# Kernel optimization log

Measured on AMD Instinct MI355X. Metric: run time of the kernel, lower is better.

Reference implementation:

```python
import jax, jax.numpy as jnp
import numpy as np

B, S, H = 32, 512, 1024


def setup_inputs() -> dict:
    key = jax.random.key(0)
    ks = jax.random.split(key, 8)
    scale = 1.0 / np.sqrt(H)
    x = jax.random.normal(ks[0], (B, S, H), dtype=jnp.float32)
    # realistic padding: each sequence has a valid length in [S//2, S]; 1 = masked
    lengths = jax.random.randint(ks[1], (B,), S // 2, S + 1)
    padding_mask = (jnp.arange(S)[None, :] >= lengths[:, None]).astype(jnp.float32)
    def w(k, shape):
        return (jax.random.normal(k, shape, dtype=jnp.float32) * scale).astype(jnp.float32)
    W_fw = w(ks[2], (H, 4 * H))
    U_fw = w(ks[3], (H, 4 * H))
    b_fw = jnp.zeros((4 * H,), jnp.float32)
    W_bw = w(ks[4], (H, 4 * H))
    U_bw = w(ks[5], (H, 4 * H))
    b_bw = jnp.zeros((4 * H,), jnp.float32)
    return {"src_token_embeddings": x, "padding_mask": padding_mask,
            "W_fw": W_fw, "U_fw": U_fw, "b_fw": b_fw,
            "W_bw": W_bw, "U_bw": U_bw, "b_bw": b_bw}


def _lstm_dir(x, mask, W, U, b):
    """Masked LSTM over time (Keras semantics: masked steps carry state and
    repeat the previous output). x: [B,S,H], mask: [B,S] with 1 = keep."""
    Bx, Sx, Hx = x.shape
    xz = jnp.einsum('bsh,hg->bsg', x, W) + b          # [B,S,4H] precomputed input gates
    xz_t = jnp.transpose(xz, (1, 0, 2))               # [S,B,4H]
    m_t = jnp.transpose(mask, (1, 0))[:, :, None]     # [S,B,1]
    h0 = jnp.zeros((Bx, Hx), x.dtype)

    def step(carry, inp):
        h, c, out_prev = carry
        z, m = inp
        z = z + h @ U                                  # [B,4H]
        i, f, g, o = jnp.split(z, 4, axis=-1)
        i = jax.nn.sigmoid(i)
        f = jax.nn.sigmoid(f)
        g = jnp.tanh(g)
        o = jax.nn.sigmoid(o)
        c_new = f * c + i * g
        h_new = o * jnp.tanh(c_new)
        h2 = m * h_new + (1.0 - m) * h
        c2 = m * c_new + (1.0 - m) * c
        out = m * h_new + (1.0 - m) * out_prev
        return (h2, c2, out), out

    (hT, cT, _), outs = jax.lax.scan(step, (h0, h0, h0), (xz_t, m_t))
    return jnp.transpose(outs, (1, 0, 2)), hT, cT


def reference(src_token_embeddings, padding_mask, W_fw, U_fw, b_fw, W_bw, U_bw, b_bw):
    x = src_token_embeddings
    mask = 1.0 - padding_mask                          # 1 = keep, as in the Keras call
    out_fw, h_fw, c_fw = _lstm_dir(x, mask, W_fw, U_fw, b_fw)
    # backward direction: process time-reversed sequence, then reverse outputs back
    out_bw_rev, h_bw, c_bw = _lstm_dir(x[:, ::-1], mask[:, ::-1], W_bw, U_bw, b_bw)
    out_bw = out_bw_rev[:, ::-1]
    encoder_outputs = jnp.concatenate([out_fw, out_bw], axis=-1)  # [B,S,2H]
    return encoder_outputs, h_fw, c_fw, h_bw, c_bw
```

## Files before the change

kernel.cpp:

```cpp
#include <hip/hip_runtime.h>
#include <hip/hip_bf16.h>

#define B 32
#define S 512
#define H 1024
#define G 4096
#define NBLK 256
#define HSLOT 65536

typedef __attribute__((ext_vector_type(8))) short bf16x8;
typedef __attribute__((ext_vector_type(8))) unsigned short u16x8;
typedef __attribute__((ext_vector_type(4))) float f32x4;

__device__ __forceinline__ unsigned short f2bf(float v) {
    __hip_bfloat16 b = __float2bfloat16(v);
    return *reinterpret_cast<unsigned short*>(&b);
}
__device__ __forceinline__ float bf2f(unsigned short u) {
    union { float f; unsigned int i; } v; v.i = ((unsigned int)u) << 16; return v.f;
}
#define MFMA(a, b, c) __builtin_amdgcn_mfma_f32_16x16x32_bf16(a, b, c, 0, 0, 0)
#define ALOAD(p)    __hip_atomic_load((p),  __ATOMIC_RELAXED, __HIP_MEMORY_SCOPE_AGENT)
#define ASTORE(p,v) __hip_atomic_store((p), (v), __ATOMIC_RELAXED, __HIP_MEMORY_SCOPE_AGENT)

__global__ __launch_bounds__(256)
void prep_weights(const float* __restrict__ fw, const float* __restrict__ bw,
                  unsigned short* __restrict__ dst)
{
    size_t idx = (size_t)blockIdx.x * 256 + threadIdx.x;
    int lane = idx & 63;
    int f    = (idx >> 6) & 15;
    int w    = (idx >> 10) & 3;
    int blk  = (int)(idx >> 12);
    int dir  = blk >> 7, jg = blk & 127;
    int ks = f >> 1, ct = f & 1;

    int c  = ct * 16 + (lane & 15);
    int g  = (c >> 3) * H + jg * 8 + (c & 7);
    int kk = w * 256 + ks * 32 + ((lane >> 4) * 8);

    const float* src = dir ? bw : fw;
    u16x8 o;
#pragma unroll
    for (int i = 0; i < 8; ++i)
        o[i] = f2bf(src[(size_t)(kk + i) * G + g]);
    *(u16x8*)&dst[idx * 8] = o;
}

__global__ __launch_bounds__(256)
void prep_x(const float* __restrict__ x, unsigned short* __restrict__ xbf)
{
    size_t i8 = ((size_t)blockIdx.x * 256 + threadIdx.x) * 8;
    float4 v0 = *(const float4*)&x[i8];
    float4 v1 = *(const float4*)&x[i8 + 4];
    u16x8 o;
    o[0] = f2bf(v0.x); o[1] = f2bf(v0.y); o[2] = f2bf(v0.z); o[3] = f2bf(v0.w);
    o[4] = f2bf(v1.x); o[5] = f2bf(v1.y); o[6] = f2bf(v1.z); o[7] = f2bf(v1.w);
    *(u16x8*)&xbf[i8] = o;
}

__global__ __launch_bounds__(512, 1)
void lstm_persist(const unsigned short* __restrict__ wbufU,
                  const unsigned short* __restrict__ wbufW,
                  const unsigned short* __restrict__ xbf,
                  unsigned short* __restrict__ hhist,
                  unsigned int* __restrict__ flags,
                  unsigned int* __restrict__ gen,
                  const float* __restrict__ pad,
                  const float* __restrict__ bfw, const float* __restrict__ bbw,
                  float* __restrict__ dout)
{
    const int blk = blockIdx.x;
    const int dir = blk >> 7;
    const int jg  = blk & 127;
    const int j0  = jg * 8;
    const int tid = threadIdx.x;
    const int wave = tid >> 6;
    const int lane = tid & 63;
    const bool is_master = (jg == 0);

    __shared__ short Uw[32768];
    __shared__ float red[4][2][16][33];
    __shared__ unsigned short ring[8][32][36];
    __shared__ unsigned rcnt;
    __shared__ unsigned gcnt;
    __shared__ unsigned tok;
    __shared__ int ring_ready[8];

    if (tid == 0) { rcnt = 0; gcnt = 0; tok = 0; }
    if (tid < 8) ring_ready[tid] = 0;
    __syncthreads();

    const int arow  = lane & 15;
    const int akoff = (lane >> 4) * 8;
    const int drow  = (lane >> 4) * 4;
    const int dcol  = lane & 15;
    const float* bsrc = dir ? bbw : bfw;
    const float wb0 = bsrc[(dcol >> 3) * H + j0 + (dcol & 7)];
    const float wb1 = bsrc[(((16 + dcol) >> 3)) * H + j0 + ((16 + dcol) & 7)];

    if (wave < 4) {
        {
            const unsigned short* src = wbufU + (((size_t)blk * 4 + wave) * 16) * 512 + lane * 8;
#pragma unroll
            for (int f = 0; f < 16; ++f)
                *(u16x8*)&Uw[((wave * 16 + f) * 64 + lane) * 8] = *(const u16x8*)(src + f * 512);
        }

        float hst = 0.f, cst = 0.f;
        const int gb  = (tid >> 3) & 31;
        const int gj  = tid & 7;
        const int gbt = gb >> 4, grow = gb & 15;
        const f32x4 zero4 = {0.f, 0.f, 0.f, 0.f};

        for (int t = 0; t < S; ++t) {
            const int s = dir ? (S - 1 - t) : t;
            float pv = pad[gb * S + s];

            if (t) {
                if (wave == 0) {
                    if (is_master) {
                        const unsigned* fb = flags + (size_t)dir * 128 * 16;
                        bool allok;
                        do {
                            unsigned v0 = ALOAD(&fb[(lane * 2 + 0) * 16]);
                            unsigned v1 = ALOAD(&fb[(lane * 2 + 1) * 16]);
                            allok = __all(v0 >= (unsigned)t && v1 >= (unsigned)t);
                            if (!allok) __builtin_amdgcn_s_sleep(1);
                        } while (!allok);
                        if (lane == 0) ASTORE(&gen[dir * 32], (unsigned)t);
                    } else {
                        while (ALOAD(&gen[dir * 32]) < (unsigned)t)
                            __builtin_amdgcn_s_sleep(1);
                    }
                    asm volatile("" ::: "memory");
                    if (lane == 0) *(volatile unsigned*)&tok = (unsigned)t;
                } else {
                    while (*(volatile unsigned*)&tok < (unsigned)t) {}
                }
                asm volatile("" ::: "memory");
            }

            f32x4 u00 = zero4, u01 = zero4, u10 = zero4, u11 = zero4;
            const unsigned short* hb = hhist + (size_t)t * HSLOT
                                     + ((size_t)(dir * B) + arow) * H + wave * 256 + akoff;
#pragma unroll
            for (int ks = 0; ks < 8; ++ks) {
                bf16x8 a0 = *(const bf16x8*)(hb + ks * 32);
                bf16x8 a1 = *(const bf16x8*)(hb + 16 * H + ks * 32);
                bf16x8 b0 = *(const bf16x8*)&Uw[((wave * 16 + ks * 2 + 0) * 64 + lane) * 8];
                bf16x8 b1 = *(const bf16x8*)&Uw[((wave * 16 + ks * 2 + 1) * 64 + lane) * 8];
                u00 = MFMA(a0, b0, u00); u01 = MFMA(a0, b1, u01);
                u10 = MFMA(a1, b0, u10); u11 = MFMA(a1, b1, u11);
            }
#pragma unroll
            for (int r = 0; r < 4; ++r) {
                red[wave][0][drow + r][dcol]      = u00[r];
                red[wave][0][drow + r][16 + dcol] = u01[r];
                red[wave][1][drow + r][dcol]      = u10[r];
                red[wave][1][drow + r][16 + dcol] = u11[r];
            }
            asm volatile("s_waitcnt lgkmcnt(0)" ::: "memory");
            if (lane == 0) atomicAdd(&rcnt, 1u);
            {
                const unsigned need = 4u * (unsigned)(t + 1);
                while (*(volatile unsigned*)&rcnt < need) {}
                asm volatile("" ::: "memory");
            }

            while (*(volatile int*)&ring_ready[t & 7] < t + 1) {}
            asm volatile("" ::: "memory");

            float z[4];
#pragma unroll
            for (int q = 0; q < 4; ++q) {
                const int c = q * 8 + gj;
                float zz = bf2f(ring[t & 7][gb][c]);
#pragma unroll
                for (int w = 0; w < 4; ++w) zz += red[w][gbt][grow][c];
                z[q] = zz;
            }
            float ig = 1.f / (1.f + expf(-z[0]));
            float fg = 1.f / (1.f + expf(-z[1]));
            float gg = tanhf(z[2]);
            float og = 1.f / (1.f + expf(-z[3]));

            float m  = 1.f - pv;
            float cn = fg * cst + ig * gg;
            float hn = og * tanhf(cn);
            float h2 = fmaf(m, hn - hst, hst);
            float c2 = fmaf(m, cn - cst, cst);
            hst = h2; cst = c2;

            unsigned u = (unsigned)f2bf(h2);
            const int gl = lane & ~3;
            unsigned v0 = (unsigned)__shfl((int)u, gl + 0);
            unsigned v1 = (unsigned)__shfl((int)u, gl + 1);
            unsigned v2 = (unsigned)__shfl((int)u, gl + 2);
            unsigned v3 = (unsigned)__shfl((int)u, gl + 3);
            if ((lane & 3) == 0) {
                unsigned long long pk = (unsigned long long)(v0 & 0xffffu)
                                      | ((unsigned long long)(v1 & 0xffffu) << 16)
                                      | ((unsigned long long)(v2 & 0xffffu) << 32)
                                      | ((unsigned long long)(v3 & 0xffffu) << 48);
                unsigned long long* hp = (unsigned long long*)
                    (hhist + (size_t)(t + 1) * HSLOT
                           + ((size_t)(dir * B) + gb) * H + j0 + gj);
                ASTORE(hp, pk);
            }
            asm volatile("s_waitcnt vmcnt(0)" ::: "memory");
            if (lane == 0) {
                unsigned old = atomicAdd(&gcnt, 1u);
                if (old == 4u * (unsigned)t + 3u)
                    ASTORE(&flags[(size_t)blk * 16], (unsigned)(t + 1));
            }

            dout[((size_t)gb * S + s) * (2 * H) + dir * H + j0 + gj] = h2;
            if (t == S - 1) {
                size_t base = (size_t)B * S * 2 * H;
                dout[base + dir * 2 * B * H + gb * H + j0 + gj] = h2;
                dout[base + dir * 2 * B * H + B * H + gb * H + j0 + gj] = c2;
            }
        }
    } else {
        const f32x4 zero4 = {0.f, 0.f, 0.f, 0.f};
        for (int fs = wave - 4; fs < S; fs += 4) {
            if (fs >= 8) {
                const unsigned need = 4u * (unsigned)(fs - 7);
                while (*(volatile unsigned*)&gcnt < need)
                    __builtin_amdgcn_s_sleep(2);
                asm volatile("" ::: "memory");
            }
            const int s2 = dir ? (S - 1 - fs) : fs;
            f32x4 a00 = zero4, a01 = zero4, a10 = zero4, a11 = zero4;
            for (int sl = 0; sl < 4; ++sl) {
                const unsigned short* wbase =
                    wbufW + (((size_t)blk * 4 + sl) * 16) * 512 + lane * 8;
                bf16x8 wf[16];
#pragma unroll
                for (int f = 0; f < 16; ++f) wf[f] = *(const bf16x8*)(wbase + f * 512);
                const unsigned short* A0 =
                    xbf + ((size_t)arow * S + s2) * H + sl * 256 + akoff;
#pragma unroll
                for (int ks = 0; ks < 8; ++ks) {
                    bf16x8 x0 = *(const bf16x8*)(A0 + ks * 32);
                    bf16x8 x1 = *(const bf16x8*)(A0 + (size_t)16 * S * H + ks * 32);
                    a00 = MFMA(x0, wf[ks*2+0], a00); a01 = MFMA(x0, wf[ks*2+1], a01);
                    a10 = MFMA(x1, wf[ks*2+0], a10); a11 = MFMA(x1, wf[ks*2+1], a11);
                }
            }
            const int slot = fs & 7;
#pragma unroll
            for (int r = 0; r < 4; ++r) {
                ring[slot][drow + r][dcol]           = f2bf(a00[r] + wb0);
                ring[slot][drow + r][16 + dcol]      = f2bf(a01[r] + wb1);
                ring[slot][16 + drow + r][dcol]      = f2bf(a10[r] + wb0);
                ring[slot][16 + drow + r][16 + dcol] = f2bf(a11[r] + wb1);
            }
            asm volatile("s_waitcnt lgkmcnt(0)" ::: "memory");
            if (lane == 0) *(volatile int*)&ring_ready[slot] = fs + 1;
        }
    }
}

extern "C" void kernel_launch(void* const* d_in, const int* in_sizes, int n_in,
                              void* d_out, int out_size, void* d_ws, size_t ws_size,
                              hipStream_t stream)
{
    const float* x   = (const float*)d_in[0];
    const float* pad = (const float*)d_in[1];
    const float* Wfw = (const float*)d_in[2];
    const float* Ufw = (const float*)d_in[3];
    const float* bfw = (const float*)d_in[4];
    const float* Wbw = (const float*)d_in[5];
    const float* Ubw = (const float*)d_in[6];
    const float* bbw = (const float*)d_in[7];
    float* out = (float*)d_out;

    char* w = (char*)d_ws;
    unsigned short* wbufW = (unsigned short*)w;
    unsigned short* wbufU = wbufW + (size_t)1048576 * 8;
    unsigned short* xbf   = wbufU + (size_t)1048576 * 8;
    unsigned short* hhist = xbf + (size_t)B * S * H;
    unsigned int*   flags = (unsigned int*)(hhist + (size_t)(S + 1) * HSLOT);
    unsigned int*   gen   = flags + 256 * 16;

    hipMemsetAsync(hhist, 0, (size_t)HSLOT * sizeof(unsigned short), stream);
    hipMemsetAsync(flags, 0, (256 * 16 + 64) * sizeof(unsigned int), stream);

    prep_x<<<8192, 256, 0, stream>>>(x, xbf);
    prep_weights<<<4096, 256, 0, stream>>>(Wfw, Wbw, wbufW);
    prep_weights<<<4096, 256, 0, stream>>>(Ufw, Ubw, wbufU);

    void* args[] = { (void*)&wbufU, (void*)&wbufW, (void*)&xbf, (void*)&hhist,
                     (void*)&flags, (void*)&gen, (void*)&pad,
                     (void*)&bfw, (void*)&bbw, (void*)&out };
    hipLaunchCooperativeKernel((void*)lstm_persist, dim3(NBLK), dim3(512),
                               args, 0, stream);
}
```

Measured before the change: 3.358 ms.

## Replace master-relayed grid barrier with per-wave polling of producer flags

Each step used to run a two-hop barrier per direction: a master block polled all 128 producer flags, published a generation counter, every block polled that counter, and wave 0 relayed it to the other waves through an LDS token. Now each compute wave polls directly and without sleeping only the 32 producer flags whose h columns it reads for its K slice. The flags are packed densely instead of padded to one per 64 bytes. This is meant to remove a global round trip and an intra-block relay from the serial per-timestep critical path. The cost is more concurrent global polling traffic on shared cache lines, with no backoff.

```diff
diff --git a/kernel.cpp b/kernel.cpp
--- a/kernel.cpp
+++ b/kernel.cpp
@@ -65,7 +65,6 @@
                   const unsigned short* __restrict__ xbf,
                   unsigned short* __restrict__ hhist,
                   unsigned int* __restrict__ flags,
-                  unsigned int* __restrict__ gen,
                   const float* __restrict__ pad,
                   const float* __restrict__ bfw, const float* __restrict__ bbw,
                   float* __restrict__ dout)
@@ -77,17 +76,15 @@
     const int tid = threadIdx.x;
     const int wave = tid >> 6;
     const int lane = tid & 63;
-    const bool is_master = (jg == 0);
 
     __shared__ short Uw[32768];
     __shared__ float red[4][2][16][33];
     __shared__ unsigned short ring[8][32][36];
     __shared__ unsigned rcnt;
     __shared__ unsigned gcnt;
-    __shared__ unsigned tok;
     __shared__ int ring_ready[8];
 
-    if (tid == 0) { rcnt = 0; gcnt = 0; tok = 0; }
+    if (tid == 0) { rcnt = 0; gcnt = 0; }
     if (tid < 8) ring_ready[tid] = 0;
     __syncthreads();
 
@@ -112,32 +109,18 @@
         const int gj  = tid & 7;
         const int gbt = gb >> 4, grow = gb & 15;
         const f32x4 zero4 = {0.f, 0.f, 0.f, 0.f};
+        const unsigned* fb = flags + (size_t)dir * 128 + wave * 32;
 
         for (int t = 0; t < S; ++t) {
             const int s = dir ? (S - 1 - t) : t;
             float pv = pad[gb * S + s];
 
             if (t) {
-                if (wave == 0) {
-                    if (is_master) {
-                        const unsigned* fb = flags + (size_t)dir * 128 * 16;
-                        bool allok;
-                        do {
-                            unsigned v0 = ALOAD(&fb[(lane * 2 + 0) * 16]);
-                            unsigned v1 = ALOAD(&fb[(lane * 2 + 1) * 16]);
-                            allok = __all(v0 >= (unsigned)t && v1 >= (unsigned)t);
-                            if (!allok) __builtin_amdgcn_s_sleep(1);
-                        } while (!allok);
-                        if (lane == 0) ASTORE(&gen[dir * 32], (unsigned)t);
-                    } else {
-                        while (ALOAD(&gen[dir * 32]) < (unsigned)t)
-                            __builtin_amdgcn_s_sleep(1);
-                    }
-                    asm volatile("" ::: "memory");
-                    if (lane == 0) *(volatile unsigned*)&tok = (unsigned)t;
-                } else {
-                    while (*(volatile unsigned*)&tok < (unsigned)t) {}
-                }
+                bool ok;
+                do {
+                    unsigned v = (lane < 32) ? ALOAD(&fb[lane]) : 0xffffffffu;
+                    ok = __all(v >= (unsigned)t);
+                } while (!ok);
                 asm volatile("" ::: "memory");
             }
 
@@ -212,7 +195,7 @@
             if (lane == 0) {
                 unsigned old = atomicAdd(&gcnt, 1u);
                 if (old == 4u * (unsigned)t + 3u)
-                    ASTORE(&flags[(size_t)blk * 16], (unsigned)(t + 1));
+                    ASTORE(&flags[(size_t)dir * 128 + jg], (unsigned)(t + 1));
             }
 
             dout[((size_t)gb * S + s) * (2 * H) + dir * H + j0 + gj] = h2;
@@ -283,17 +266,16 @@
     unsigned short* xbf   = wbufU + (size_t)1048576 * 8;
     unsigned short* hhist = xbf + (size_t)B * S * H;
     unsigned int*   flags = (unsigned int*)(hhist + (size_t)(S + 1) * HSLOT);
-    unsigned int*   gen   = flags + 256 * 16;
 
     hipMemsetAsync(hhist, 0, (size_t)HSLOT * sizeof(unsigned short), stream);
-    hipMemsetAsync(flags, 0, (256 * 16 + 64) * sizeof(unsigned int), stream);
+    hipMemsetAsync(flags, 0, 256 * sizeof(unsigned int), stream);
 
     prep_x<<<8192, 256, 0, stream>>>(x, xbf);
     prep_weights<<<4096, 256, 0, stream>>>(Wfw, Wbw, wbufW);
     prep_weights<<<4096, 256, 0, stream>>>(Ufw, Ubw, wbufU);
 
     void* args[] = { (void*)&wbufU, (void*)&wbufW, (void*)&xbf, (void*)&hhist,
-                     (void*)&flags, (void*)&gen, (void*)&pad,
+                     (void*)&flags, (void*)&pad,
                      (void*)&bfw, (void*)&bbw, (void*)&out };
     hipLaunchCooperativeKernel((void*)lstm_persist, dim3(NBLK), dim3(512),
                                args, 0, stream);
```

After: 4.757 ms. 41.6% more time.
